# Kernel optimization log

Hardware: AMD Instinct MI355X
Metric: run time of the kernel (lower is better)

## Reference

```python
import jax, jax.numpy as jnp
import numpy as np

B, C, H, W = 32, 64, 32, 32
N = H * W  # 1024 spatial positions


def setup_inputs() -> dict:
    key = jax.random.key(0)
    ks = jax.random.split(key, 7)
    s_c = 1.0 / np.sqrt(C)
    s_n = 1.0 / np.sqrt(N)
    return {
        "x": jax.random.normal(ks[0], (B, C, H, W), dtype=jnp.float32),
        "w_phi": jax.random.normal(ks[1], (C, C), dtype=jnp.float32) * s_c,
        "w_theta": jax.random.normal(ks[2], (C, C), dtype=jnp.float32) * s_c,
        "w_g": jax.random.normal(ks[3], (C, C), dtype=jnp.float32) * s_c,
        "w_mask": jax.random.normal(ks[4], (C, C), dtype=jnp.float32) * s_c,
        "w_mv": jax.random.normal(ks[5], (C, C), dtype=jnp.float32) * s_c,
        "w_mk": jax.random.normal(ks[6], (N, N), dtype=jnp.float32) * s_n,
    }


def reference(x, w_phi, w_theta, w_g, w_mask, w_mv, w_mk):
    b, c, h, w = x.shape
    n = h * w
    xf = x.reshape(b, c, n)  # [b, c, N]
    # 1x1 convs == channel GEMMs (weight layout [out, in])
    phi = jnp.einsum("oc,bcn->bon", w_phi, xf)      # [b, c, N]
    theta = jnp.einsum("oc,bcn->bno", w_theta, xf)  # [b, N, c]
    g = jnp.einsum("oc,bcn->bno", w_g, xf)          # [b, N, c]
    # mv: Linear(c, c) on last dim of g  (y = g @ W^T)
    g = jnp.einsum("bnc,dc->bnd", g, w_mv)
    # theta @ phi -> [b, N, N]
    att = jnp.einsum("bnc,bcm->bnm", theta, phi)
    # mk: Linear(N, N) on last dim
    att = jnp.einsum("bnm,km->bnk", att, w_mk)
    # softmax over dim=1 (rows of the NxN map)
    att = jax.nn.softmax(att, axis=1)
    # att @ g -> [b, N, c]
    out = jnp.einsum("bnm,bmc->bnc", att, g)
    out = out.transpose(0, 2, 1).reshape(b, c, h, w)
    mask = jnp.einsum("oc,bchw->bohw", w_mask, out)
    return mask + x
```

## Files before the change

### kernel.cpp

```cpp
#include <hip/hip_runtime.h>

#define BB 32
#define CC 64
#define NN 1024

typedef __attribute__((ext_vector_type(8))) short bf8;
typedef __attribute__((ext_vector_type(4))) float f4;
typedef __attribute__((ext_vector_type(4))) unsigned short us4;

__device__ __forceinline__ unsigned short f2bf(float f) {
    unsigned u = __float_as_uint(f);
    return (unsigned short)((u + 0x7fffu + ((u >> 16) & 1u)) >> 16);
}
__device__ __forceinline__ float bf2f(unsigned short u) {
    return __uint_as_float(((unsigned)u) << 16);
}

#define MFMA(a, b, c) __builtin_amdgcn_mfma_f32_16x16x32_bf16(a, b, c, 0, 0, 0)

#define GLDS(g, l)                                                              \
    __builtin_amdgcn_global_load_lds(                                           \
        (const __attribute__((address_space(1))) void*)(g),                     \
        (__attribute__((address_space(3))) void*)(l), 16, 0, 0)

__device__ __forceinline__ void swz512(int i, int& b, int& t0) {
    int gid = (i & 7) * 64 + (i >> 3);
    b = gid >> 4;
    t0 = (gid & 15) * 64;
}

__global__ void k0_prep(const float* __restrict__ w_mv, const float* __restrict__ w_g,
                        const float* __restrict__ w_theta, const float* __restrict__ w_phi,
                        const float* __restrict__ w_mask, const float* __restrict__ w_mk,
                        unsigned short* __restrict__ wcat_bf,
                        unsigned short* __restrict__ wmask_bf,
                        unsigned short* __restrict__ wmk_bf) {
    int tid = threadIdx.x;
    if (blockIdx.x < 1024) {
        int i = (blockIdx.x * 256 + tid) * 4;
        float4 v = *(const float4*)(w_mk + i);
        us4 r;
        r.x = f2bf(v.x); r.y = f2bf(v.y); r.z = f2bf(v.z); r.w = f2bf(v.w);
        *(us4*)(wmk_bf + i) = r;
    } else {
        int idx = (blockIdx.x - 1024) * 256 + tid;
        int d = idx >> 6, e = idx & 63;
        float acc = 0.f;
        for (int c = 0; c < 64; ++c) acc += w_mv[d * 64 + c] * w_g[c * 64 + e];
        wcat_bf[idx] = f2bf(w_theta[idx]);
        wcat_bf[4096 + idx] = f2bf(w_phi[idx]);
        wcat_bf[8192 + idx] = f2bf(acc);
        wmask_bf[idx] = f2bf(w_mask[idx]);
    }
}

__global__ __launch_bounds__(256, 4) void k1_channel(const float* __restrict__ x,
                                                     const unsigned short* __restrict__ wcat,
                                                     unsigned short* __restrict__ theta_nc,
                                                     unsigned short* __restrict__ phi_cm,
                                                     unsigned short* __restrict__ g2_cm) {
    __shared__ unsigned short xT[64][66];
    int b = blockIdx.y;
    int n0 = blockIdx.x * 64;
    int tid = threadIdx.x;
    int w = tid >> 6, lane = tid & 63, l16 = lane & 15, q = lane >> 4;
    size_t bo = (size_t)b * CC * NN;
#pragma unroll
    for (int i = 0; i < 16; ++i) {
        int idx = i * 256 + tid;
        int c = idx >> 6, n2 = idx & 63;
        xT[n2][c] = f2bf(x[bo + (size_t)c * NN + n0 + n2]);
    }
    __syncthreads();
    bf8 bF[4][2];
#pragma unroll
    for (int ct = 0; ct < 4; ++ct) {
        bF[ct][0] = *(const bf8*)&xT[ct * 16 + l16][q * 8];
        bF[ct][1] = *(const bf8*)&xT[ct * 16 + l16][32 + q * 8];
    }
#pragma unroll
    for (int rt = 0; rt < 3; ++rt) {
        int R = w * 48 + rt * 16;
        const unsigned short* wa = wcat + (R + l16) * 64 + q * 8;
        bf8 a0 = *(const bf8*)wa;
        bf8 a1 = *(const bf8*)(wa + 32);
        int which = R >> 6, rb = R & 63;
#pragma unroll
        for (int ct = 0; ct < 4; ++ct) {
            f4 acc = {0.f, 0.f, 0.f, 0.f};
            acc = MFMA(a0, bF[ct][0], acc);
            acc = MFMA(a1, bF[ct][1], acc);
            int n = n0 + ct * 16 + l16;
            if (which == 0) {
                us4 t;
                t.x = f2bf(acc[0]); t.y = f2bf(acc[1]);
                t.z = f2bf(acc[2]); t.w = f2bf(acc[3]);
                *(us4*)&theta_nc[bo + (size_t)n * 64 + rb + q * 4] = t;
            } else {
                unsigned short* dst = (which == 1 ? phi_cm : g2_cm) + bo;
#pragma unroll
                for (int r = 0; r < 4; ++r)
                    dst[(size_t)(rb + q * 4 + r) * NN + n] = f2bf(acc[r]);
            }
        }
    }
}

__global__ __launch_bounds__(512, 4) void k2_phi2(const unsigned short* __restrict__ phi_cm,
                                                  const unsigned short* __restrict__ wmk_bf,
                                                  unsigned short* __restrict__ phi2t) {
    __shared__ __align__(16) unsigned short bT[2][4096];
    int b, k0;
    swz512(blockIdx.x, b, k0);
    int tid = threadIdx.x;
    int w = tid >> 6, lane = tid & 63, l16 = lane & 15, q = lane >> 4;
    int ks = w & 3, ch = w >> 2;
    size_t bo = (size_t)b * CC * NN;
    int srow = w * 8 + (lane >> 3);
    int scol = ((lane & 7) ^ (lane >> 3)) * 8;
    const unsigned short* gsrc = phi_cm + bo + (size_t)srow * NN + scol;
    const unsigned short* arow = wmk_bf + (size_t)(k0 + ks * 16 + l16) * NN + q * 8;
    f4 acc[2];
    acc[0] = (f4){0.f, 0.f, 0.f, 0.f};
    acc[1] = (f4){0.f, 0.f, 0.f, 0.f};
    bf8 aC0 = *(const bf8*)(arow);
    bf8 aC1 = *(const bf8*)(arow + 32);
    GLDS(gsrc, &bT[0][w * 512]);
    __syncthreads();
#pragma unroll 2
    for (int mc = 0; mc < 16; ++mc) {
        const unsigned short* bTc = bT[mc & 1];
        bf8 aN0 = aC0, aN1 = aC1;
        if (mc < 15) {
            int mn = (mc + 1) * 64;
            aN0 = *(const bf8*)(arow + mn);
            aN1 = *(const bf8*)(arow + mn + 32);
            GLDS(gsrc + mn, &bT[(mc + 1) & 1][w * 512]);
            asm volatile("s_waitcnt vmcnt(3)" ::: "memory");
        } else {
            asm volatile("s_waitcnt vmcnt(0)" ::: "memory");
        }
        __builtin_amdgcn_s_barrier();
        __builtin_amdgcn_sched_barrier(0);
#pragma unroll
        for (int t = 0; t < 2; ++t) {
            int row = (ch * 2 + t) * 16 + l16;
            int sw = (row & 7) * 8;
            bf8 b0 = *(const bf8*)&bTc[row * 64 + ((q * 8) ^ sw)];
            bf8 b1 = *(const bf8*)&bTc[row * 64 + ((32 + q * 8) ^ sw)];
            acc[t] = MFMA(aC0, b0, acc[t]);
            acc[t] = MFMA(aC1, b1, acc[t]);
        }
        __builtin_amdgcn_s_barrier();
        __builtin_amdgcn_sched_barrier(0);
        aC0 = aN0;
        aC1 = aN1;
    }
    unsigned short* prow = phi2t + bo;
#pragma unroll
    for (int t = 0; t < 2; ++t) {
        int ccol = (ch * 2 + t) * 16 + l16;
#pragma unroll
        for (int r = 0; r < 4; ++r)
            prow[(size_t)(k0 + ks * 16 + q * 4 + r) * 64 + ccol] = f2bf(acc[t][r]);
    }
}

__global__ __launch_bounds__(512, 4) void k3_stats(const unsigned short* __restrict__ theta_nc,
                                                   const unsigned short* __restrict__ phi2t,
                                                   float* __restrict__ sinv) {
    __shared__ float sred[8][64];
    int b, k0;
    swz512(blockIdx.x, b, k0);
    int tid = threadIdx.x;
    int w = tid >> 6, lane = tid & 63, l16 = lane & 15, q = lane >> 4;
    int wq = w & 3, nh = w >> 2;
    size_t bo = (size_t)b * CC * NN;
    bf8 bF[4][2];
#pragma unroll
    for (int tc = 0; tc < 4; ++tc)
#pragma unroll
        for (int kc = 0; kc < 2; ++kc)
            bF[tc][kc] = *(const bf8*)(phi2t + bo + (size_t)(k0 + tc * 16 + l16) * 64 + kc * 32 + q * 8);
    float s[4] = {0.f, 0.f, 0.f, 0.f};
    const unsigned short* thb = theta_nc + bo + q * 8;
    int nbase = nh * 8;
    int nrow0 = (nbase + 0) * 64 + wq * 16 + l16;
    bf8 a0 = *(const bf8*)(thb + (size_t)nrow0 * 64);
    bf8 a1 = *(const bf8*)(thb + (size_t)nrow0 * 64 + 32);
    for (int nb = 0; nb < 8; ++nb) {
        bf8 p0, p1;
        if (nb < 7) {
            int nr = (nbase + nb + 1) * 64 + wq * 16 + l16;
            p0 = *(const bf8*)(thb + (size_t)nr * 64);
            p1 = *(const bf8*)(thb + (size_t)nr * 64 + 32);
        }
#pragma unroll
        for (int tc = 0; tc < 4; ++tc) {
            f4 acc = {0.f, 0.f, 0.f, 0.f};
            acc = MFMA(a0, bF[tc][0], acc);
            acc = MFMA(a1, bF[tc][1], acc);
            s[tc] += __expf(acc[0]) + __expf(acc[1]) + __expf(acc[2]) + __expf(acc[3]);
        }
        a0 = p0;
        a1 = p1;
    }
#pragma unroll
    for (int tc = 0; tc < 4; ++tc) {
        s[tc] += __shfl_xor(s[tc], 16, 64);
        s[tc] += __shfl_xor(s[tc], 32, 64);
    }
    if (q == 0) {
#pragma unroll
        for (int tc = 0; tc < 4; ++tc) sred[w][tc * 16 + l16] = s[tc];
    }
    __syncthreads();
    if (tid < 64) {
        float S = 0.f;
#pragma unroll
        for (int ww = 0; ww < 8; ++ww) S += sred[ww][tid];
        sinv[(size_t)b * NN + k0 + tid] = 1.f / S;
    }
}

__global__ __launch_bounds__(512, 4) void k4_out(const unsigned short* __restrict__ theta_nc,
                                                 const unsigned short* __restrict__ phi2t,
                                                 const unsigned short* __restrict__ g2_cm,
                                                 const float* __restrict__ sinv,
                                                 const unsigned short* __restrict__ wmask_bf,
                                                 const float* __restrict__ x,
                                                 float* __restrict__ out) {
    __shared__ __align__(16) unsigned short smem[23040];
    float* svs_l = (float*)(smem + 20992);
    int b, n0;
    swz512(blockIdx.x, b, n0);
    int tid = threadIdx.x;
    int w = tid >> 6, lane = tid & 63, l16 = lane & 15, q = lane >> 4;
    int ws = w & 3, ph = w >> 2;
    int nl = ws * 16 + l16;
    size_t bo = (size_t)b * CC * NN;
    int srow = w * 8 + (lane >> 3);
    int scol = ((lane & 7) ^ (lane >> 3)) * 8;
    const unsigned short* p2b = phi2t + bo;
    const unsigned short* g2b = g2_cm + bo;
    if (tid < 256) *(f4*)&svs_l[tid * 4] = *(const f4*)(sinv + (size_t)b * NN + tid * 4);
    bf8 thB[2];
#pragma unroll
    for (int kc = 0; kc < 2; ++kc)
        thB[kc] = *(const bf8*)(theta_nc + bo + (size_t)(n0 + nl) * 64 + kc * 32 + q * 8);
    f4 accO[4];
#pragma unroll
    for (int ct = 0; ct < 4; ++ct) accO[ct] = (f4){0.f, 0.f, 0.f, 0.f};
    GLDS(p2b + (size_t)srow * 64 + scol, smem + w * 512);
    GLDS(g2b + (size_t)srow * NN + scol, smem + 4096 + w * 512);
    __syncthreads();
#pragma unroll 2
    for (int mc = 0; mc < 16; ++mc) {
        unsigned short* aT = smem + (mc & 1) * 8192;
        unsigned short* gT = aT + 4096;
        if (mc < 15) {
            int mn = (mc + 1) * 64;
            unsigned short* aN = smem + ((mc + 1) & 1) * 8192;
            GLDS(p2b + (size_t)(mn + srow) * 64 + scol, aN + w * 512);
            GLDS(g2b + (size_t)srow * NN + mn + scol, aN + 4096 + w * 512);
            asm volatile("s_waitcnt vmcnt(2)" ::: "memory");
        } else {
            asm volatile("s_waitcnt vmcnt(0)" ::: "memory");
        }
        __builtin_amdgcn_s_barrier();
        __builtin_amdgcn_sched_barrier(0);
        int m0 = mc * 64;
        unsigned short* Pr = smem + 16384 + nl * 72 + ph * 32;
        int swz = (l16 & 7) * 8;
#pragma unroll
        for (int mrr = 0; mrr < 2; ++mrr) {
            int rowA = ph * 32 + mrr * 16 + l16;
            bf8 a0 = *(const bf8*)&aT[rowA * 64 + ((q * 8) ^ swz)];
            bf8 a1 = *(const bf8*)&aT[rowA * 64 + ((32 + q * 8) ^ swz)];
            f4 at = {0.f, 0.f, 0.f, 0.f};
            at = MFMA(a0, thB[0], at);
            at = MFMA(a1, thB[1], at);
            f4 sv = *(const f4*)&svs_l[m0 + ph * 32 + mrr * 16 + q * 4];
            us4 pk;
            pk.x = f2bf(__expf(at[0]) * sv[0]);
            pk.y = f2bf(__expf(at[1]) * sv[1]);
            pk.z = f2bf(__expf(at[2]) * sv[2]);
            pk.w = f2bf(__expf(at[3]) * sv[3]);
            *(us4*)&Pr[mrr * 16 + q * 4] = pk;
        }
        bf8 pF = *(const bf8*)&Pr[q * 8];
#pragma unroll
        for (int ct = 0; ct < 4; ++ct) {
            int rowG = ct * 16 + l16;
            bf8 g0 = *(const bf8*)&gT[rowG * 64 + (((ph * 32) + q * 8) ^ swz)];
            accO[ct] = MFMA(g0, pF, accO[ct]);
        }
        __builtin_amdgcn_s_barrier();
        __builtin_amdgcn_sched_barrier(0);
    }
    float* o_red = (float*)smem;
    unsigned short* o_lds = smem + 8704;
    if (ph == 1) {
#pragma unroll
        for (int ct = 0; ct < 4; ++ct)
#pragma unroll
            for (int r = 0; r < 4; ++r) o_red[(ct * 16 + q * 4 + r) * 68 + nl] = accO[ct][r];
    }
    __syncthreads();
    if (ph == 0) {
#pragma unroll
        for (int ct = 0; ct < 4; ++ct) {
            us4 ov;
            ov.x = f2bf(accO[ct][0] + o_red[(ct * 16 + q * 4 + 0) * 68 + nl]);
            ov.y = f2bf(accO[ct][1] + o_red[(ct * 16 + q * 4 + 1) * 68 + nl]);
            ov.z = f2bf(accO[ct][2] + o_red[(ct * 16 + q * 4 + 2) * 68 + nl]);
            ov.w = f2bf(accO[ct][3] + o_red[(ct * 16 + q * 4 + 3) * 68 + nl]);
            *(us4*)&o_lds[nl * 72 + ct * 16 + q * 4] = ov;
        }
    }
    __syncthreads();
    bf8 oB0 = *(const bf8*)&o_lds[nl * 72 + q * 8];
    bf8 oB1 = *(const bf8*)&o_lds[nl * 72 + 32 + q * 8];
#pragma unroll
    for (int t2 = 0; t2 < 2; ++t2) {
        int tr = ph * 2 + t2;
        const unsigned short* wa = wmask_bf + (tr * 16 + l16) * 64 + q * 8;
        bf8 w0 = *(const bf8*)wa;
        bf8 w1 = *(const bf8*)(wa + 32);
        f4 accF = {0.f, 0.f, 0.f, 0.f};
        accF = MFMA(w0, oB0, accF);
        accF = MFMA(w1, oB1, accF);
#pragma unroll
        for (int r = 0; r < 4; ++r) {
            size_t ix = bo + (size_t)(tr * 16 + q * 4 + r) * NN + n0 + nl;
            out[ix] = accF[r] + x[ix];
        }
    }
}

extern "C" void kernel_launch(void* const* d_in, const int* in_sizes, int n_in,
                              void* d_out, int out_size, void* d_ws, size_t ws_size,
                              hipStream_t stream) {
    const float* x       = (const float*)d_in[0];
    const float* w_phi   = (const float*)d_in[1];
    const float* w_theta = (const float*)d_in[2];
    const float* w_g     = (const float*)d_in[3];
    const float* w_mask  = (const float*)d_in[4];
    const float* w_mv    = (const float*)d_in[5];
    const float* w_mk    = (const float*)d_in[6];
    float* out = (float*)d_out;

    const size_t CN = (size_t)BB * CC * NN;
    char* p = (char*)d_ws;
    unsigned short* theta_nc = (unsigned short*)p; p += CN * 2;
    unsigned short* phi_cm = (unsigned short*)p;   p += CN * 2;
    unsigned short* g2_cm = (unsigned short*)p;    p += CN * 2;
    float* sinv = (float*)p;                       p += CN * 2;
    unsigned short* phi2t = (unsigned short*)p;    p += CN * 2;
    unsigned short* wmk_bf = (unsigned short*)p;   p += (size_t)NN * NN * 2;
    unsigned short* wcat_bf = (unsigned short*)p;  p += 192 * 64 * 2;
    unsigned short* wmask_bf = (unsigned short*)p; p += 4096 * 2;

    k0_prep<<<1040, 256, 0, stream>>>(w_mv, w_g, w_theta, w_phi, w_mask, w_mk,
                                      wcat_bf, wmask_bf, wmk_bf);
    k1_channel<<<dim3(16, BB), 256, 0, stream>>>(x, wcat_bf, theta_nc, phi_cm, g2_cm);
    k2_phi2<<<512, 512, 0, stream>>>(phi_cm, wmk_bf, phi2t);
    k3_stats<<<512, 512, 0, stream>>>(theta_nc, phi2t, sinv);
    k4_out<<<512, 512, 0, stream>>>(theta_nc, phi2t, g2_cm, sinv, wmask_bf, x, out);
}
```

Before: 134.9 us.

## Fuse phi2 GEMM with softmax column stats and halve channel-kernel tile

Merges the phi·W_mk GEMM kernel and the softmax-denominator kernel into one launch. The phi2 tile is kept in shared memory and reused directly, and theta tiles are streamed through the double-buffered LDS via async global-to-LDS loads. Separately, the channel-GEMM kernel now uses 32-position tiles with float4 loads, doubling the grid. This removes one kernel launch and a phi2 round trip through global memory, at the cost of more LDS per block and a longer serial loop in the fused kernel.

```diff
diff --git a/kernel.cpp b/kernel.cpp
--- a/kernel.cpp
+++ b/kernel.cpp
@@ -59,22 +59,26 @@
                                                      unsigned short* __restrict__ theta_nc,
                                                      unsigned short* __restrict__ phi_cm,
                                                      unsigned short* __restrict__ g2_cm) {
-    __shared__ unsigned short xT[64][66];
+    __shared__ __align__(16) unsigned short xT[32][72];
     int b = blockIdx.y;
-    int n0 = blockIdx.x * 64;
+    int n0 = blockIdx.x * 32;
     int tid = threadIdx.x;
     int w = tid >> 6, lane = tid & 63, l16 = lane & 15, q = lane >> 4;
     size_t bo = (size_t)b * CC * NN;
 #pragma unroll
-    for (int i = 0; i < 16; ++i) {
-        int idx = i * 256 + tid;
-        int c = idx >> 6, n2 = idx & 63;
-        xT[n2][c] = f2bf(x[bo + (size_t)c * NN + n0 + n2]);
-    }
-    __syncthreads();
-    bf8 bF[4][2];
-#pragma unroll
-    for (int ct = 0; ct < 4; ++ct) {
+    for (int i = 0; i < 2; ++i) {
+        int f = i * 1024 + tid * 4;
+        int c = f >> 5, n = f & 31;
+        float4 v = *(const float4*)(x + bo + (size_t)c * NN + n0 + n);
+        xT[n + 0][c] = f2bf(v.x);
+        xT[n + 1][c] = f2bf(v.y);
+        xT[n + 2][c] = f2bf(v.z);
+        xT[n + 3][c] = f2bf(v.w);
+    }
+    __syncthreads();
+    bf8 bF[2][2];
+#pragma unroll
+    for (int ct = 0; ct < 2; ++ct) {
         bF[ct][0] = *(const bf8*)&xT[ct * 16 + l16][q * 8];
         bF[ct][1] = *(const bf8*)&xT[ct * 16 + l16][32 + q * 8];
     }
@@ -86,7 +90,7 @@
         bf8 a1 = *(const bf8*)(wa + 32);
         int which = R >> 6, rb = R & 63;
 #pragma unroll
-        for (int ct = 0; ct < 4; ++ct) {
+        for (int ct = 0; ct < 2; ++ct) {
             f4 acc = {0.f, 0.f, 0.f, 0.f};
             acc = MFMA(a0, bF[ct][0], acc);
             acc = MFMA(a1, bF[ct][1], acc);
@@ -106,18 +110,24 @@
     }
 }
 
-__global__ __launch_bounds__(512, 4) void k2_phi2(const unsigned short* __restrict__ phi_cm,
-                                                  const unsigned short* __restrict__ wmk_bf,
-                                                  unsigned short* __restrict__ phi2t) {
+__global__ __launch_bounds__(512, 4) void k23_phi2_stats(
+    const unsigned short* __restrict__ phi_cm,
+    const unsigned short* __restrict__ wmk_bf,
+    const unsigned short* __restrict__ theta_nc,
+    unsigned short* __restrict__ phi2t,
+    float* __restrict__ sinv) {
     __shared__ __align__(16) unsigned short bT[2][4096];
+    __shared__ __align__(16) unsigned short pT[64][72];
+    __shared__ float sred[8][32];
     int b, k0;
     swz512(blockIdx.x, b, k0);
     int tid = threadIdx.x;
     int w = tid >> 6, lane = tid & 63, l16 = lane & 15, q = lane >> 4;
-    int ks = w & 3, ch = w >> 2;
     size_t bo = (size_t)b * CC * NN;
     int srow = w * 8 + (lane >> 3);
     int scol = ((lane & 7) ^ (lane >> 3)) * 8;
+
+    int ks = w & 3, ch = w >> 2;
     const unsigned short* gsrc = phi_cm + bo + (size_t)srow * NN + scol;
     const unsigned short* arow = wmk_bf + (size_t)(k0 + ks * 16 + l16) * NN + q * 8;
     f4 acc[2];
@@ -161,64 +171,64 @@
     for (int t = 0; t < 2; ++t) {
         int ccol = (ch * 2 + t) * 16 + l16;
 #pragma unroll
-        for (int r = 0; r < 4; ++r)
-            prow[(size_t)(k0 + ks * 16 + q * 4 + r) * 64 + ccol] = f2bf(acc[t][r]);
-    }
-}
-
-__global__ __launch_bounds__(512, 4) void k3_stats(const unsigned short* __restrict__ theta_nc,
-                                                   const unsigned short* __restrict__ phi2t,
-                                                   float* __restrict__ sinv) {
-    __shared__ float sred[8][64];
-    int b, k0;
-    swz512(blockIdx.x, b, k0);
-    int tid = threadIdx.x;
-    int w = tid >> 6, lane = tid & 63, l16 = lane & 15, q = lane >> 4;
-    int wq = w & 3, nh = w >> 2;
-    size_t bo = (size_t)b * CC * NN;
-    bf8 bF[4][2];
-#pragma unroll
-    for (int tc = 0; tc < 4; ++tc)
+        for (int r = 0; r < 4; ++r) {
+            int krow = ks * 16 + q * 4 + r;
+            unsigned short v = f2bf(acc[t][r]);
+            pT[krow][ccol] = v;
+            prow[(size_t)(k0 + krow) * 64 + ccol] = v;
+        }
+    }
+
+    int rg = w & 3, th = w >> 2;
+    const unsigned short* thsrc = theta_nc + bo + (size_t)srow * 64 + scol;
+    GLDS(thsrc, &bT[0][w * 512]);
+    __syncthreads();
+    bf8 pF[2][2];
+#pragma unroll
+    for (int t = 0; t < 2; ++t)
 #pragma unroll
         for (int kc = 0; kc < 2; ++kc)
-            bF[tc][kc] = *(const bf8*)(phi2t + bo + (size_t)(k0 + tc * 16 + l16) * 64 + kc * 32 + q * 8);
-    float s[4] = {0.f, 0.f, 0.f, 0.f};
-    const unsigned short* thb = theta_nc + bo + q * 8;
-    int nbase = nh * 8;
-    int nrow0 = (nbase + 0) * 64 + wq * 16 + l16;
-    bf8 a0 = *(const bf8*)(thb + (size_t)nrow0 * 64);
-    bf8 a1 = *(const bf8*)(thb + (size_t)nrow0 * 64 + 32);
-    for (int nb = 0; nb < 8; ++nb) {
-        bf8 p0, p1;
-        if (nb < 7) {
-            int nr = (nbase + nb + 1) * 64 + wq * 16 + l16;
-            p0 = *(const bf8*)(thb + (size_t)nr * 64);
-            p1 = *(const bf8*)(thb + (size_t)nr * 64 + 32);
-        }
-#pragma unroll
-        for (int tc = 0; tc < 4; ++tc) {
-            f4 acc = {0.f, 0.f, 0.f, 0.f};
-            acc = MFMA(a0, bF[tc][0], acc);
-            acc = MFMA(a1, bF[tc][1], acc);
-            s[tc] += __expf(acc[0]) + __expf(acc[1]) + __expf(acc[2]) + __expf(acc[3]);
-        }
-        a0 = p0;
-        a1 = p1;
-    }
-#pragma unroll
-    for (int tc = 0; tc < 4; ++tc) {
-        s[tc] += __shfl_xor(s[tc], 16, 64);
-        s[tc] += __shfl_xor(s[tc], 32, 64);
+            pF[t][kc] = *(const bf8*)&pT[(th * 2 + t) * 16 + l16][kc * 32 + q * 8];
+    float s[2] = {0.f, 0.f};
+#pragma unroll 2
+    for (int nc = 0; nc < 16; ++nc) {
+        const unsigned short* tTc = bT[nc & 1];
+        if (nc < 15) {
+            GLDS(thsrc + (nc + 1) * 4096, &bT[(nc + 1) & 1][w * 512]);
+            asm volatile("s_waitcnt vmcnt(1)" ::: "memory");
+        } else {
+            asm volatile("s_waitcnt vmcnt(0)" ::: "memory");
+        }
+        __builtin_amdgcn_s_barrier();
+        __builtin_amdgcn_sched_barrier(0);
+        int r = rg * 16 + l16;
+        int sw = (r & 7);
+        bf8 a0 = *(const bf8*)&tTc[r * 64 + ((q ^ sw) * 8)];
+        bf8 a1 = *(const bf8*)&tTc[r * 64 + (((4 + q) ^ sw) * 8)];
+#pragma unroll
+        for (int t = 0; t < 2; ++t) {
+            f4 at = {0.f, 0.f, 0.f, 0.f};
+            at = MFMA(a0, pF[t][0], at);
+            at = MFMA(a1, pF[t][1], at);
+            s[t] += __expf(at[0]) + __expf(at[1]) + __expf(at[2]) + __expf(at[3]);
+        }
+        __builtin_amdgcn_s_barrier();
+        __builtin_amdgcn_sched_barrier(0);
+    }
+#pragma unroll
+    for (int t = 0; t < 2; ++t) {
+        s[t] += __shfl_xor(s[t], 16, 64);
+        s[t] += __shfl_xor(s[t], 32, 64);
     }
     if (q == 0) {
-#pragma unroll
-        for (int tc = 0; tc < 4; ++tc) sred[w][tc * 16 + l16] = s[tc];
+        sred[w][l16] = s[0];
+        sred[w][16 + l16] = s[1];
     }
     __syncthreads();
     if (tid < 64) {
-        float S = 0.f;
-#pragma unroll
-        for (int ww = 0; ww < 8; ++ww) S += sred[ww][tid];
+        int th2 = tid >> 5, rem = tid & 31;
+        float S = sred[th2 * 4 + 0][rem] + sred[th2 * 4 + 1][rem] +
+                  sred[th2 * 4 + 2][rem] + sred[th2 * 4 + 3][rem];
         sinv[(size_t)b * NN + k0 + tid] = 1.f / S;
     }
 }
@@ -363,8 +373,7 @@
 
     k0_prep<<<1040, 256, 0, stream>>>(w_mv, w_g, w_theta, w_phi, w_mask, w_mk,
                                       wcat_bf, wmask_bf, wmk_bf);
-    k1_channel<<<dim3(16, BB), 256, 0, stream>>>(x, wcat_bf, theta_nc, phi_cm, g2_cm);
-    k2_phi2<<<512, 512, 0, stream>>>(phi_cm, wmk_bf, phi2t);
-    k3_stats<<<512, 512, 0, stream>>>(theta_nc, phi2t, sinv);
+    k1_channel<<<dim3(32, BB), 256, 0, stream>>>(x, wcat_bf, theta_nc, phi_cm, g2_cm);
+    k23_phi2_stats<<<512, 512, 0, stream>>>(phi_cm, wmk_bf, theta_nc, phi2t, sinv);
     k4_out<<<512, 512, 0, stream>>>(theta_nc, phi2t, g2_cm, sinv, wmask_bf, x, out);
 }
```

Measured after the change: 131.7 us. 2.4% less time.
